# Kernel optimization log

Hardware: AMD Instinct MI355X
Metric: run time of the kernel (lower is better)

## Reference

```python
import jax, jax.numpy as jnp
import numpy as np

N_NODES = 50000

def _spmm(edge_index, edge_weight, feat):
    # adj @ feat where adj is given as COO edge list (dst <- src)
    src = edge_index[1]
    dst = edge_index[0]
    msgs = feat[src] * edge_weight[:, None]  # [E, F]
    return jax.ops.segment_sum(msgs, dst, num_segments=N_NODES)

def setup_inputs() -> dict:
    key = jax.random.key(0)
    ks = jax.random.split(key, 8)
    E = 1600000
    x = jax.random.normal(ks[0], (N_NODES, 512), dtype=jnp.float32)
    edge_index = jax.random.randint(ks[1], (2, E), 0, N_NODES, dtype=jnp.int32)
    edge_weight = jax.random.uniform(ks[2], (E,), dtype=jnp.float32)
    # Glorot-ish init like GraphConvolution.reset_parameters
    W1 = jax.random.normal(ks[3], (512, 128), dtype=jnp.float32) / np.sqrt(512)
    b1 = jax.random.normal(ks[4], (128,), dtype=jnp.float32) * 0.01
    W2 = jax.random.normal(ks[5], (128, 64), dtype=jnp.float32) / np.sqrt(128)
    b2 = jax.random.normal(ks[6], (64,), dtype=jnp.float32) * 0.01
    return {"x": x, "edge_index": edge_index, "edge_weight": edge_weight,
            "W1": W1, "b1": b1, "W2": W2, "b2": b2}

def reference(x, edge_index, edge_weight, W1, b1, W2, b2):
    # eval mode: F.dropout is identity when not training
    # gc1: adj @ (x @ W1) + b1, then relu
    support1 = x @ W1                                   # [N, nhid]
    x1 = jax.nn.relu(_spmm(edge_index, edge_weight, support1) + b1)
    # gc2: adj @ (x1 @ W2) + b2
    support2 = x1 @ W2                                  # [N, out]
    x2 = _spmm(edge_index, edge_weight, support2) + b2
    return (x1, x2)
```

## Files before the change

### kernel.cpp

```cpp
#include <hip/hip_runtime.h>
#include <hip/hip_bf16.h>

#define N_NODES 50000
#define N_EDGES 1600000
#define F_IN    512
#define F_HID   128
#define F_OUT   64
#define NBUK    391
#define EPB     8192
#define CAP     4864

typedef short bf16x8 __attribute__((ext_vector_type(8)));
typedef float f32x4  __attribute__((ext_vector_type(4)));

__device__ __forceinline__ short f32_to_bf16(float f) {
    unsigned u = __float_as_uint(f);
    u += 0x7FFF + ((u >> 16) & 1);
    return (short)(u >> 16);
}
__device__ __forceinline__ float bf16_to_f32(short s) {
    return __uint_as_float(((unsigned)(unsigned short)s) << 16);
}
__device__ __forceinline__ float bf16lo(unsigned u) { return __uint_as_float(u << 16); }
__device__ __forceinline__ float bf16hi(unsigned u) { return __uint_as_float(u & 0xFFFF0000u); }


__global__ __launch_bounds__(256) void part_a(const int* __restrict__ dst,
                                              const int* __restrict__ src,
                                              const float* __restrict__ w,
                                              int* __restrict__ gcnt,
                                              uint2* __restrict__ tmp, int E) {
    __shared__ int h[NBUK];
    __shared__ int base[NBUK];
    for (int i = threadIdx.x; i < NBUK; i += 256) h[i] = 0;
    __syncthreads();
    int e0 = blockIdx.x * EPB;
    int e1 = min(e0 + EPB, E);
    for (int e = e0 + threadIdx.x; e < e1; e += 256)
        atomicAdd(&h[dst[e] >> 7], 1);
    __syncthreads();
    for (int i = threadIdx.x; i < NBUK; i += 256) {
        int c = h[i];
        base[i] = c ? atomicAdd(&gcnt[i], c) : 0;
        h[i] = 0;
    }
    __syncthreads();
    for (int e = e0 + threadIdx.x; e < e1; e += 256) {
        int d = dst[e];
        int b = d >> 7;
        int off = base[b] + atomicAdd(&h[b], 1);
        if (off < CAP)
            tmp[(size_t)b * CAP + off] = make_uint2(((unsigned)d << 16) | (unsigned)src[e],
                                                    __float_as_uint(w[e]));
    }
}

__global__ __launch_bounds__(256) void part_b(const uint2* __restrict__ tmp,
                                              const int* __restrict__ gcnt,
                                              int2* __restrict__ rowinfo,
                                              uint2* __restrict__ erec) {
    __shared__ int s[128];
    __shared__ int cur[128];
    int b = blockIdx.x, tid = threadIdx.x;
    int nb0 = b << 7;
    int r0 = b * CAP;
    int cnt_b = min(gcnt[b], CAP);
    int r1 = r0 + cnt_b;
    if (tid < 128) s[tid] = 0;
    __syncthreads();
    for (int i = r0 + tid; i < r1; i += 256)
        atomicAdd(&s[(tmp[i].x >> 16) - nb0], 1);
    __syncthreads();
    int v = (tid < 128) ? s[tid] : 0;
    #pragma unroll
    for (int off = 1; off < 128; off <<= 1) {
        int t = (tid >= off && tid < 128) ? s[tid - off] : 0;
        __syncthreads();
        if (tid < 128) s[tid] += t;
        __syncthreads();
    }
    if (tid < 128) {
        int ex = r0 + s[tid] - v;
        cur[tid] = ex;
        int node = nb0 + tid;
        if (node < N_NODES) rowinfo[node] = make_int2(ex, ex + v);
    }
    __syncthreads();
    for (int i = r0 + tid; i < r1; i += 256) {
        uint2 rec = tmp[i];
        int p = atomicAdd(&cur[(rec.x >> 16) - nb0], 1);
        erec[p] = make_uint2(rec.x & 0xFFFFu, rec.y);
    }
}


template<int KD>
__global__ __launch_bounds__(256) void cvt_frag(const float* __restrict__ X,
                                                bf16x8* __restrict__ Afrag, int n_units) {
    constexpr int KC = KD / 32;
    int u = blockIdx.x * 256 + threadIdx.x;
    if (u >= n_units) return;
    int lane = u & 63;
    int kc   = (u >> 6) & (KC - 1);
    int tile = u / (64 * KC);
    int row  = tile * 16 + (lane & 15);
    int k    = kc * 32 + (lane >> 4) * 8;
    const float* p = X + (size_t)row * KD + k;
    float4 a0 = *(const float4*)p;
    float4 a1 = *(const float4*)(p + 4);
    bf16x8 f;
    f[0] = f32_to_bf16(a0.x); f[1] = f32_to_bf16(a0.y);
    f[2] = f32_to_bf16(a0.z); f[3] = f32_to_bf16(a0.w);
    f[4] = f32_to_bf16(a1.x); f[5] = f32_to_bf16(a1.y);
    f[6] = f32_to_bf16(a1.z); f[7] = f32_to_bf16(a1.w);
    Afrag[u] = f;
}

template<int KD, int NC>
__global__ void wtrans_frag(const float* __restrict__ W, bf16x8* __restrict__ Bfrag) {
    constexpr int KC = KD / 32, NT = NC / 16;
    int u = blockIdx.x * 256 + threadIdx.x;
    if (u >= KC * NT * 64) return;
    int lane = u & 63;
    int nt   = (u >> 6) % NT;
    int kc   = u / (64 * NT);
    int n = nt * 16 + (lane & 15);
    int k = kc * 32 + (lane >> 4) * 8;
    bf16x8 f;
    #pragma unroll
    for (int j = 0; j < 8; ++j) f[j] = f32_to_bf16(W[(size_t)(k + j) * NC + n]);
    Bfrag[u] = f;
}


template<int NC, int KD>
__global__ __launch_bounds__(256) void mfma_gemm_frag(const bf16x8* __restrict__ Afrag,
                                                      const bf16x8* __restrict__ Bfrag,
                                                      short* __restrict__ C, int Mt) {
    constexpr int NT = NC / 16, KC = KD / 32;
    constexpr int PFA = (KC < 4) ? KC : 4;
    const int lane = threadIdx.x & 63;
    const int wave = threadIdx.x >> 6;
    const int tile = blockIdx.x * 4 + wave;
    if (tile >= Mt) return;

    const bf16x8* ap = Afrag + (size_t)tile * KC * 64 + lane;
    const bf16x8* bp = Bfrag + lane;

    f32x4 acc[NT];
    #pragma unroll
    for (int i = 0; i < NT; ++i) acc[i] = (f32x4){0.f, 0.f, 0.f, 0.f};

    bf16x8 abuf[PFA];
    #pragma unroll
    for (int i = 0; i < PFA; ++i) abuf[i] = ap[(size_t)i * 64];
    bf16x8 bbuf[NT];
    #pragma unroll
    for (int nt = 0; nt < NT; ++nt) bbuf[nt] = bp[(size_t)nt * 64];

    #pragma unroll
    for (int kc = 0; kc < KC; ++kc) {
        bf16x8 a = abuf[kc % PFA];
        int ka = kc + PFA; if (ka > KC - 1) ka = KC - 1;
        abuf[kc % PFA] = ap[(size_t)ka * 64];
        int kb = (kc + 1 < KC) ? kc + 1 : kc;
        bf16x8 bnew[NT];
        #pragma unroll
        for (int nt = 0; nt < NT; ++nt) {
            bnew[nt] = bp[((size_t)kb * NT + nt) * 64];
            acc[nt] = __builtin_amdgcn_mfma_f32_16x16x32_bf16(a, bbuf[nt], acc[nt], 0, 0, 0);
        }
        #pragma unroll
        for (int nt = 0; nt < NT; ++nt) bbuf[nt] = bnew[nt];
    }

    const int lrow = lane & 15, kgrp = lane >> 4;
    #pragma unroll
    for (int nt = 0; nt < NT; ++nt) {
        #pragma unroll
        for (int r = 0; r < 4; ++r) {
            int grow = tile * 16 + kgrp * 4 + r;
            C[(size_t)grow * NC + nt * 16 + lrow] = f32_to_bf16(acc[nt][r]);
        }
    }
}


__global__ __launch_bounds__(64) void spmm128(const int2* __restrict__ rowinfo,
                                              const uint2* __restrict__ erec,
                                              const unsigned* __restrict__ featu,
                                              const float* __restrict__ bias,
                                              float* __restrict__ out,
                                              unsigned* __restrict__ afrag2u) {
    int d = blockIdx.x, tid = threadIdx.x;
    int2 ri = rowinfo[d];
    int beg = ri.x, end = ri.y;
    float a0 = 0.f, a1 = 0.f;
    int e = beg;
    for (; e + 4 <= end; e += 4) {
        uint2 r0 = erec[e], r1 = erec[e + 1], r2 = erec[e + 2], r3 = erec[e + 3];
        unsigned f0 = featu[(size_t)r0.x * 64 + tid];
        unsigned f1 = featu[(size_t)r1.x * 64 + tid];
        unsigned f2 = featu[(size_t)r2.x * 64 + tid];
        unsigned f3 = featu[(size_t)r3.x * 64 + tid];
        float w0 = __uint_as_float(r0.y), w1 = __uint_as_float(r1.y);
        float w2 = __uint_as_float(r2.y), w3 = __uint_as_float(r3.y);
        a0 += w0 * bf16lo(f0); a1 += w0 * bf16hi(f0);
        a0 += w1 * bf16lo(f1); a1 += w1 * bf16hi(f1);
        a0 += w2 * bf16lo(f2); a1 += w2 * bf16hi(f2);
        a0 += w3 * bf16lo(f3); a1 += w3 * bf16hi(f3);
    }
    for (; e < end; ++e) {
        uint2 r = erec[e];
        unsigned f = featu[(size_t)r.x * 64 + tid];
        float w = __uint_as_float(r.y);
        a0 += w * bf16lo(f); a1 += w * bf16hi(f);
    }
    float ox = fmaxf(a0 + bias[2 * tid], 0.f);
    float oy = fmaxf(a1 + bias[2 * tid + 1], 0.f);
    *(float2*)&out[(size_t)d * 128 + 2 * tid] = make_float2(ox, oy);
    unsigned packed = (unsigned)(unsigned short)f32_to_bf16(ox) |
                      ((unsigned)(unsigned short)f32_to_bf16(oy) << 16);
    int unit = ((d >> 4) * 4 + (tid >> 4)) * 64 + ((tid >> 2) & 3) * 16 + (d & 15);
    afrag2u[unit * 4 + (tid & 3)] = packed;
}

__global__ __launch_bounds__(64) void spmm64(const int2* __restrict__ rowinfo,
                                             const uint2* __restrict__ erec,
                                             const short* __restrict__ feat,
                                             const float* __restrict__ bias,
                                             float* __restrict__ out) {
    int d = blockIdx.x, tid = threadIdx.x;
    int2 ri = rowinfo[d];
    int beg = ri.x, end = ri.y;
    float acc = 0.f;
    int e = beg;
    for (; e + 4 <= end; e += 4) {
        uint2 r0 = erec[e], r1 = erec[e + 1], r2 = erec[e + 2], r3 = erec[e + 3];
        float f0 = bf16_to_f32(feat[(size_t)r0.x * 64 + tid]);
        float f1 = bf16_to_f32(feat[(size_t)r1.x * 64 + tid]);
        float f2 = bf16_to_f32(feat[(size_t)r2.x * 64 + tid]);
        float f3 = bf16_to_f32(feat[(size_t)r3.x * 64 + tid]);
        acc += __uint_as_float(r0.y) * f0;
        acc += __uint_as_float(r1.y) * f1;
        acc += __uint_as_float(r2.y) * f2;
        acc += __uint_as_float(r3.y) * f3;
    }
    for (; e < end; ++e) {
        uint2 r = erec[e];
        acc += __uint_as_float(r.y) * bf16_to_f32(feat[(size_t)r.x * 64 + tid]);
    }
    out[(size_t)d * 64 + tid] = acc + bias[tid];
}


extern "C" void kernel_launch(void* const* d_in, const int* in_sizes, int n_in,
                              void* d_out, int out_size, void* d_ws, size_t ws_size,
                              hipStream_t stream) {
    const float* x  = (const float*)d_in[0];
    const int*   ei = (const int*)d_in[1];
    const float* ew = (const float*)d_in[2];
    const float* W1 = (const float*)d_in[3];
    const float* b1 = (const float*)d_in[4];
    const float* W2 = (const float*)d_in[5];
    const float* b2 = (const float*)d_in[6];

    const int* dst = ei;
    const int* src = ei + N_EDGES;

    float* x1 = (float*)d_out;
    float* x2 = x1 + (size_t)N_NODES * F_HID;

    char* ws = (char*)d_ws;
    uint2*  erec     = (uint2*)ws;  ws += (size_t)NBUK * CAP * 8;
    uint2*  tmp      = (uint2*)ws;  ws += (size_t)NBUK * CAP * 8;
    short*  support1 = (short*)ws;  ws += (size_t)N_NODES * F_HID * 2;
    short*  support2 = (short*)ws;  ws += (size_t)N_NODES * F_OUT * 2;
    bf16x8* Afrag1   = (bf16x8*)ws; ws += (size_t)N_NODES * F_IN * 2;
    bf16x8* Afrag2   = (bf16x8*)ws; ws += (size_t)N_NODES * F_HID * 2;
    bf16x8* Bfrag1   = (bf16x8*)ws; ws += (size_t)F_HID * F_IN * 2;
    bf16x8* Bfrag2   = (bf16x8*)ws; ws += (size_t)F_OUT * F_HID * 2;
    int2*   rowinfo  = (int2*)ws;   ws += (size_t)N_NODES * 8;
    int*    gcnt     = (int*)ws;    ws += 400 * 4;

    const int NPB = (N_EDGES + EPB - 1) / EPB;
    const int MT  = N_NODES / 16;

    {
        int n_units = MT * (F_IN / 32) * 64;
        cvt_frag<F_IN><<<(n_units + 255) / 256, 256, 0, stream>>>(x, Afrag1, n_units);
    }

    hipMemsetAsync(gcnt, 0, NBUK * sizeof(int), stream);
    part_a<<<NPB, 256, 0, stream>>>(dst, src, ew, gcnt, tmp, N_EDGES);
    part_b<<<NBUK, 256, 0, stream>>>(tmp, gcnt, rowinfo, erec);

    wtrans_frag<F_IN, F_HID><<<32, 256, 0, stream>>>(W1, Bfrag1);
    wtrans_frag<F_HID, F_OUT><<<4, 256, 0, stream>>>(W2, Bfrag2);

    mfma_gemm_frag<F_HID, F_IN><<<(MT + 3) / 4, 256, 0, stream>>>(Afrag1, Bfrag1, support1, MT);

    spmm128<<<N_NODES, 64, 0, stream>>>(rowinfo, erec, (const unsigned*)support1, b1, x1,
                                        (unsigned*)Afrag2);

    mfma_gemm_frag<F_OUT, F_HID><<<(MT + 3) / 4, 256, 0, stream>>>(Afrag2, Bfrag2, support2, MT);

    spmm64<<<N_NODES, 64, 0, stream>>>(rowinfo, erec, support2, b2, x2);
}
```

Baseline: 375.0 us.

## Chunk support features by column, compress edge records, split SpMM over feature chunks

The GEMM now writes its support outputs in column-chunked layout (32 features per chunk, contiguous per node). The SpMM kernels gain a grid dimension over chunks so each chunk table (about 3.2MB for layer 1) is more likely to stay in cache during random gathers, and a wave handles 4 edges in parallel with 16 lanes per edge followed by a shuffle reduction. Edge records shrink from 8 to 4 bytes by packing the 16-bit src index with a bf16 weight, and nontemporal loads and stores are used for the streaming arrays. The cost is that edge records are re-read once per chunk, edge weights lose precision, and the wave reduction adds some overhead.

```diff
diff --git a/kernel.cpp b/kernel.cpp
--- a/kernel.cpp
+++ b/kernel.cpp
@@ -12,15 +12,14 @@
 
 typedef short bf16x8 __attribute__((ext_vector_type(8)));
 typedef float f32x4  __attribute__((ext_vector_type(4)));
+typedef unsigned uintx2 __attribute__((ext_vector_type(2)));
+typedef float f32x2  __attribute__((ext_vector_type(2)));
 
 __device__ __forceinline__ short f32_to_bf16(float f) {
     unsigned u = __float_as_uint(f);
     u += 0x7FFF + ((u >> 16) & 1);
     return (short)(u >> 16);
 }
-__device__ __forceinline__ float bf16_to_f32(short s) {
-    return __uint_as_float(((unsigned)(unsigned short)s) << 16);
-}
 __device__ __forceinline__ float bf16lo(unsigned u) { return __uint_as_float(u << 16); }
 __device__ __forceinline__ float bf16hi(unsigned u) { return __uint_as_float(u & 0xFFFF0000u); }
 
@@ -29,7 +28,7 @@
                                               const int* __restrict__ src,
                                               const float* __restrict__ w,
                                               int* __restrict__ gcnt,
-                                              uint2* __restrict__ tmp, int E) {
+                                              uintx2* __restrict__ tmp, int E) {
     __shared__ int h[NBUK];
     __shared__ int base[NBUK];
     for (int i = threadIdx.x; i < NBUK; i += 256) h[i] = 0;
@@ -49,16 +48,17 @@
         int d = dst[e];
         int b = d >> 7;
         int off = base[b] + atomicAdd(&h[b], 1);
-        if (off < CAP)
-            tmp[(size_t)b * CAP + off] = make_uint2(((unsigned)d << 16) | (unsigned)src[e],
-                                                    __float_as_uint(w[e]));
-    }
-}
-
-__global__ __launch_bounds__(256) void part_b(const uint2* __restrict__ tmp,
+        if (off < CAP) {
+            uintx2 rec = { ((unsigned)d << 16) | (unsigned)src[e], __float_as_uint(w[e]) };
+            __builtin_nontemporal_store(rec, &tmp[(size_t)b * CAP + off]);
+        }
+    }
+}
+
+__global__ __launch_bounds__(256) void part_b(const uintx2* __restrict__ tmp,
                                               const int* __restrict__ gcnt,
                                               int2* __restrict__ rowinfo,
-                                              uint2* __restrict__ erec) {
+                                              unsigned* __restrict__ erec) {
     __shared__ int s[128];
     __shared__ int cur[128];
     int b = blockIdx.x, tid = threadIdx.x;
@@ -87,9 +87,10 @@
     }
     __syncthreads();
     for (int i = r0 + tid; i < r1; i += 256) {
-        uint2 rec = tmp[i];
+        uintx2 rec = __builtin_nontemporal_load(&tmp[i]);
         int p = atomicAdd(&cur[(rec.x >> 16) - nb0], 1);
-        erec[p] = make_uint2(rec.x & 0xFFFFu, rec.y);
+        unsigned wb = (unsigned)(unsigned short)f32_to_bf16(__uint_as_float(rec.y));
+        __builtin_nontemporal_store((rec.x << 16) | wb, &erec[p]);
     }
 }
 
@@ -136,7 +137,8 @@
 template<int NC, int KD>
 __global__ __launch_bounds__(256) void mfma_gemm_frag(const bf16x8* __restrict__ Afrag,
                                                       const bf16x8* __restrict__ Bfrag,
-                                                      short* __restrict__ C, int Mt) {
+                                                      short* __restrict__ Cc,
+                                                      int Mt, int M) {
     constexpr int NT = NC / 16, KC = KD / 32;
     constexpr int PFA = (KC < 4) ? KC : 4;
     const int lane = threadIdx.x & 63;
@@ -177,80 +179,80 @@
     const int lrow = lane & 15, kgrp = lane >> 4;
     #pragma unroll
     for (int nt = 0; nt < NT; ++nt) {
+        int f = nt * 16 + lrow;
+        int cch = f >> 5, slot = f & 31;
         #pragma unroll
         for (int r = 0; r < 4; ++r) {
             int grow = tile * 16 + kgrp * 4 + r;
-            C[(size_t)grow * NC + nt * 16 + lrow] = f32_to_bf16(acc[nt][r]);
+            Cc[((size_t)cch * M + grow) * 32 + slot] = f32_to_bf16(acc[nt][r]);
         }
     }
 }
 
 
-__global__ __launch_bounds__(64) void spmm128(const int2* __restrict__ rowinfo,
-                                              const uint2* __restrict__ erec,
-                                              const unsigned* __restrict__ featu,
-                                              const float* __restrict__ bias,
-                                              float* __restrict__ out,
-                                              unsigned* __restrict__ afrag2u) {
-    int d = blockIdx.x, tid = threadIdx.x;
+__global__ __launch_bounds__(256) void spmm128c(const int2* __restrict__ rowinfo,
+                                                const unsigned* __restrict__ erec,
+                                                const unsigned* __restrict__ supp1c,
+                                                const float* __restrict__ bias,
+                                                float* __restrict__ x1,
+                                                unsigned* __restrict__ afrag2u) {
+    int d = blockIdx.x * 4 + (threadIdx.x >> 6);
+    int lane = threadIdx.x & 63;
+    int es = lane >> 4, fs = lane & 15;
+    int c = blockIdx.y;
+    const unsigned* table = supp1c + (size_t)c * N_NODES * 16;
     int2 ri = rowinfo[d];
-    int beg = ri.x, end = ri.y;
     float a0 = 0.f, a1 = 0.f;
-    int e = beg;
-    for (; e + 4 <= end; e += 4) {
-        uint2 r0 = erec[e], r1 = erec[e + 1], r2 = erec[e + 2], r3 = erec[e + 3];
-        unsigned f0 = featu[(size_t)r0.x * 64 + tid];
-        unsigned f1 = featu[(size_t)r1.x * 64 + tid];
-        unsigned f2 = featu[(size_t)r2.x * 64 + tid];
-        unsigned f3 = featu[(size_t)r3.x * 64 + tid];
-        float w0 = __uint_as_float(r0.y), w1 = __uint_as_float(r1.y);
-        float w2 = __uint_as_float(r2.y), w3 = __uint_as_float(r3.y);
-        a0 += w0 * bf16lo(f0); a1 += w0 * bf16hi(f0);
-        a0 += w1 * bf16lo(f1); a1 += w1 * bf16hi(f1);
-        a0 += w2 * bf16lo(f2); a1 += w2 * bf16hi(f2);
-        a0 += w3 * bf16lo(f3); a1 += w3 * bf16hi(f3);
-    }
-    for (; e < end; ++e) {
-        uint2 r = erec[e];
-        unsigned f = featu[(size_t)r.x * 64 + tid];
-        float w = __uint_as_float(r.y);
+    for (int e = ri.x + es; ; e += 4) {
+        unsigned rec = 0;
+        if (e < ri.y) rec = __builtin_nontemporal_load(&erec[e]);
+        else if (e - es >= ri.y) break;
+        float w = __uint_as_float(rec << 16);
+        unsigned f = table[(size_t)(rec >> 16) * 16 + fs];
         a0 += w * bf16lo(f); a1 += w * bf16hi(f);
     }
-    float ox = fmaxf(a0 + bias[2 * tid], 0.f);
-    float oy = fmaxf(a1 + bias[2 * tid + 1], 0.f);
-    *(float2*)&out[(size_t)d * 128 + 2 * tid] = make_float2(ox, oy);
-    unsigned packed = (unsigned)(unsigned short)f32_to_bf16(ox) |
-                      ((unsigned)(unsigned short)f32_to_bf16(oy) << 16);
-    int unit = ((d >> 4) * 4 + (tid >> 4)) * 64 + ((tid >> 2) & 3) * 16 + (d & 15);
-    afrag2u[unit * 4 + (tid & 3)] = packed;
-}
-
-__global__ __launch_bounds__(64) void spmm64(const int2* __restrict__ rowinfo,
-                                             const uint2* __restrict__ erec,
-                                             const short* __restrict__ feat,
-                                             const float* __restrict__ bias,
-                                             float* __restrict__ out) {
-    int d = blockIdx.x, tid = threadIdx.x;
+    a0 += __shfl_xor(a0, 16, 64); a1 += __shfl_xor(a1, 16, 64);
+    a0 += __shfl_xor(a0, 32, 64); a1 += __shfl_xor(a1, 32, 64);
+    float ox = fmaxf(a0 + bias[32 * c + 2 * fs], 0.f);
+    float oy = fmaxf(a1 + bias[32 * c + 2 * fs + 1], 0.f);
+    if (es == 1) {
+        f32x2 o = {ox, oy};
+        __builtin_nontemporal_store(o, (f32x2*)&x1[(size_t)d * 128 + 32 * c + 2 * fs]);
+    }
+    if (es == 0) {
+        unsigned packed = (unsigned)(unsigned short)f32_to_bf16(ox) |
+                          ((unsigned)(unsigned short)f32_to_bf16(oy) << 16);
+        int uidx = (((d >> 4) * 4 + c) * 64 + ((fs >> 2) << 4) + (d & 15)) * 4 + (fs & 3);
+        __builtin_nontemporal_store(packed, &afrag2u[uidx]);
+    }
+}
+
+__global__ __launch_bounds__(256) void spmm64c(const int2* __restrict__ rowinfo,
+                                               const unsigned* __restrict__ erec,
+                                               const unsigned* __restrict__ supp2c,
+                                               const float* __restrict__ bias,
+                                               float* __restrict__ x2) {
+    int d = blockIdx.x * 4 + (threadIdx.x >> 6);
+    int lane = threadIdx.x & 63;
+    int es = lane >> 4, fs = lane & 15;
+    int c = blockIdx.y;
+    const unsigned* table = supp2c + (size_t)c * N_NODES * 16;
     int2 ri = rowinfo[d];
-    int beg = ri.x, end = ri.y;
-    float acc = 0.f;
-    int e = beg;
-    for (; e + 4 <= end; e += 4) {
-        uint2 r0 = erec[e], r1 = erec[e + 1], r2 = erec[e + 2], r3 = erec[e + 3];
-        float f0 = bf16_to_f32(feat[(size_t)r0.x * 64 + tid]);
-        float f1 = bf16_to_f32(feat[(size_t)r1.x * 64 + tid]);
-        float f2 = bf16_to_f32(feat[(size_t)r2.x * 64 + tid]);
-        float f3 = bf16_to_f32(feat[(size_t)r3.x * 64 + tid]);
-        acc += __uint_as_float(r0.y) * f0;
-        acc += __uint_as_float(r1.y) * f1;
-        acc += __uint_as_float(r2.y) * f2;
-        acc += __uint_as_float(r3.y) * f3;
-    }
-    for (; e < end; ++e) {
-        uint2 r = erec[e];
-        acc += __uint_as_float(r.y) * bf16_to_f32(feat[(size_t)r.x * 64 + tid]);
-    }
-    out[(size_t)d * 64 + tid] = acc + bias[tid];
+    float a0 = 0.f, a1 = 0.f;
+    for (int e = ri.x + es; ; e += 4) {
+        unsigned rec = 0;
+        if (e < ri.y) rec = __builtin_nontemporal_load(&erec[e]);
+        else if (e - es >= ri.y) break;
+        float w = __uint_as_float(rec << 16);
+        unsigned f = table[(size_t)(rec >> 16) * 16 + fs];
+        a0 += w * bf16lo(f); a1 += w * bf16hi(f);
+    }
+    a0 += __shfl_xor(a0, 16, 64); a1 += __shfl_xor(a1, 16, 64);
+    a0 += __shfl_xor(a0, 32, 64); a1 += __shfl_xor(a1, 32, 64);
+    if (es == 0) {
+        f32x2 o = {a0 + bias[32 * c + 2 * fs], a1 + bias[32 * c + 2 * fs + 1]};
+        __builtin_nontemporal_store(o, (f32x2*)&x2[(size_t)d * 64 + 32 * c + 2 * fs]);
+    }
 }
 
 
@@ -272,16 +274,16 @@
     float* x2 = x1 + (size_t)N_NODES * F_HID;
 
     char* ws = (char*)d_ws;
-    uint2*  erec     = (uint2*)ws;  ws += (size_t)NBUK * CAP * 8;
-    uint2*  tmp      = (uint2*)ws;  ws += (size_t)NBUK * CAP * 8;
-    short*  support1 = (short*)ws;  ws += (size_t)N_NODES * F_HID * 2;
-    short*  support2 = (short*)ws;  ws += (size_t)N_NODES * F_OUT * 2;
-    bf16x8* Afrag1   = (bf16x8*)ws; ws += (size_t)N_NODES * F_IN * 2;
-    bf16x8* Afrag2   = (bf16x8*)ws; ws += (size_t)N_NODES * F_HID * 2;
-    bf16x8* Bfrag1   = (bf16x8*)ws; ws += (size_t)F_HID * F_IN * 2;
-    bf16x8* Bfrag2   = (bf16x8*)ws; ws += (size_t)F_OUT * F_HID * 2;
-    int2*   rowinfo  = (int2*)ws;   ws += (size_t)N_NODES * 8;
-    int*    gcnt     = (int*)ws;    ws += 400 * 4;
+    unsigned* erec    = (unsigned*)ws; ws += (size_t)NBUK * CAP * 4;
+    uintx2* tmp       = (uintx2*)ws;   ws += (size_t)NBUK * CAP * 8;
+    short*  supp1c    = (short*)ws;    ws += (size_t)N_NODES * F_HID * 2;
+    short*  supp2c    = (short*)ws;    ws += (size_t)N_NODES * F_OUT * 2;
+    bf16x8* Afrag1    = (bf16x8*)ws;   ws += (size_t)N_NODES * F_IN * 2;
+    bf16x8* Afrag2    = (bf16x8*)ws;   ws += (size_t)N_NODES * F_HID * 2;
+    bf16x8* Bfrag1    = (bf16x8*)ws;   ws += (size_t)F_HID * F_IN * 2;
+    bf16x8* Bfrag2    = (bf16x8*)ws;   ws += (size_t)F_OUT * F_HID * 2;
+    int2*   rowinfo   = (int2*)ws;     ws += (size_t)N_NODES * 8;
+    int*    gcnt      = (int*)ws;      ws += 400 * 4;
 
     const int NPB = (N_EDGES + EPB - 1) / EPB;
     const int MT  = N_NODES / 16;
@@ -291,19 +293,25 @@
         cvt_frag<F_IN><<<(n_units + 255) / 256, 256, 0, stream>>>(x, Afrag1, n_units);
     }
 
-    hipMemsetAsync(gcnt, 0, NBUK * sizeof(int), stream);
+    (void)hipMemsetAsync(gcnt, 0, NBUK * sizeof(int), stream);
     part_a<<<NPB, 256, 0, stream>>>(dst, src, ew, gcnt, tmp, N_EDGES);
     part_b<<<NBUK, 256, 0, stream>>>(tmp, gcnt, rowinfo, erec);
 
     wtrans_frag<F_IN, F_HID><<<32, 256, 0, stream>>>(W1, Bfrag1);
     wtrans_frag<F_HID, F_OUT><<<4, 256, 0, stream>>>(W2, Bfrag2);
 
-    mfma_gemm_frag<F_HID, F_IN><<<(MT + 3) / 4, 256, 0, stream>>>(Afrag1, Bfrag1, support1, MT);
-
-    spmm128<<<N_NODES, 64, 0, stream>>>(rowinfo, erec, (const unsigned*)support1, b1, x1,
+    mfma_gemm_frag<F_HID, F_IN><<<(MT + 3) / 4, 256, 0, stream>>>(Afrag1, Bfrag1, supp1c, MT, N_NODES);
+
+    {
+        dim3 g(N_NODES / 4, F_HID / 32);
+        spmm128c<<<g, 256, 0, stream>>>(rowinfo, erec, (const unsigned*)supp1c, b1, x1,
                                         (unsigned*)Afrag2);
-
-    mfma_gemm_frag<F_OUT, F_HID><<<(MT + 3) / 4, 256, 0, stream>>>(Afrag2, Bfrag2, support2, MT);
-
-    spmm64<<<N_NODES, 64, 0, stream>>>(rowinfo, erec, support2, b2, x2);
-}
+    }
+
+    mfma_gemm_frag<F_OUT, F_HID><<<(MT + 3) / 4, 256, 0, stream>>>(Afrag2, Bfrag2, supp2c, MT, N_NODES);
+
+    {
+        dim3 g(N_NODES / 4, F_OUT / 32);
+        spmm64c<<<g, 256, 0, stream>>>(rowinfo, erec, (const unsigned*)supp2c, b2, x2);
+    }
+}
```

Result: slower. 629.4 us (+67.8%).
